# Kernel tuning notes

Measured on AMD Instinct MI355X. Metric: run time of the kernel, lower is better.

## Reference

```python
import jax, jax.numpy as jnp
import numpy as np

N_ATOMS = 32768
N_EDGES = 262144
ATOM_F = 256
EDGE_F = 128
OUT_F = 512
N_GAUSS = 50
SPIN_D = 3


def setup_inputs() -> dict:
    key = jax.random.key(0)
    k1, k2, k3, k4, k5 = jax.random.split(key, 5)
    h = jax.random.normal(k1, (N_ATOMS, ATOM_F), dtype=jnp.float32)
    m = jax.random.normal(k2, (N_EDGES, EDGE_F), dtype=jnp.float32)
    magft_cat = jax.random.normal(k3, (N_ATOMS, SPIN_D), dtype=jnp.float32)
    edge_index = jax.random.randint(k4, (2, N_EDGES), 0, N_ATOMS, dtype=jnp.int64)
    in_f = 2 * ATOM_F + EDGE_F + N_GAUSS  # 690
    W = jax.random.normal(k5, (OUT_F, in_f), dtype=jnp.float32) * 0.02
    return {"h": h, "m": m, "magft_cat": magft_cat, "edge_index": edge_index, "W": W}


def reference(h, m, magft_cat, edge_index, W):
    # GaussianSmearing(-1.5, 1.5, 50)
    offsets = jnp.linspace(-1.5, 1.5, N_GAUSS, dtype=jnp.float32)  # (G,)
    coeff = -0.5 / (offsets[1] - offsets[0]) ** 2

    src = edge_index[0]
    tgt = edge_index[1]
    h_s = h[src]                     # (E, A)
    h_t = h[tgt]                     # (E, A)
    # per-edge spin dot product, (E, 1)
    d = jnp.sum(magft_cat[src] * magft_cat[tgt], axis=1, keepdims=True)
    spin_edge = jnp.exp(coeff * (d - offsets) ** 2)  # (E, G)
    m_st = jnp.concatenate([h_s, h_t, m, spin_edge], axis=-1)  # (E, 690)
    # bias-free Dense with activation=None
    return m_st @ W.T  # (E, OUT_F)
```

## Files before the change

kernel.cpp:

```cpp
#include <hip/hip_runtime.h>
#include <hip/hip_bf16.h>

#define N_ATOMS 32768
#define N_EDGESC 262144
#define ATOM_F 256
#define EDGE_F 128
#define OUT_F 512
#define N_GAUSS 50
#define IN_F 690
#define NCHUNK 11

#define BM 128
#define BN 512
#define NTHREADS 512

using f32x4  = __attribute__((ext_vector_type(4))) float;
using short8 = __attribute__((ext_vector_type(8))) short;

__device__ __forceinline__ unsigned short f2bf(float f) {
  unsigned int u = __builtin_bit_cast(unsigned int, f);
  u += 0x7fffu + ((u >> 16) & 1u);
  return (unsigned short)(u >> 16);
}

__global__ void detect_idx_kernel(const unsigned int* __restrict__ ei, int* __restrict__ flag) {
  if (threadIdx.x == 0) {
    int ok = 1;
    for (int i = 0; i < 64; ++i) {
      unsigned int lo = ei[2 * i], hi = ei[2 * i + 1];
      if (hi != 0u || lo >= (unsigned)N_ATOMS) { ok = 0; break; }
    }
    *flag = ok;
  }
}

__global__ void prep_w_kernel(const float* __restrict__ W, unsigned short* __restrict__ Wp) {
  int g = blockIdx.x * blockDim.x + threadIdx.x;
  if (g >= NCHUNK * 2 * 32 * 64) return;
  int l  = g & 63;
  int nt = (g >> 6) & 31;
  int ks = (g >> 11) & 1;
  int kc = g >> 12;
  int n  = nt * 16 + (l & 15);
  int k0 = kc * 64 + ks * 32 + ((l >> 4) << 3);
  unsigned int u[4];
#pragma unroll
  for (int p = 0; p < 4; ++p) {
    int ka = k0 + 2 * p, kb = k0 + 2 * p + 1;
    float va = (ka < IN_F) ? W[n * IN_F + ka] : 0.0f;
    float vb = (kb < IN_F) ? W[n * IN_F + kb] : 0.0f;
    u[p] = (unsigned)f2bf(va) | ((unsigned)f2bf(vb) << 16);
  }
  *(uint4*)(Wp + (size_t)g * 8) = make_uint4(u[0], u[1], u[2], u[3]);
}

__global__ __launch_bounds__(NTHREADS, 2) void gemm_kernel(
    const float* __restrict__ h, const float* __restrict__ m,
    const float* __restrict__ magft, const void* __restrict__ ei,
    const int* __restrict__ flagp, const unsigned short* __restrict__ Wp,
    float* __restrict__ out)
{
  __shared__ __align__(16) unsigned short As[2][BM * 64];
  __shared__ int sIdx[BM], tIdx[BM];
  __shared__ float dLDS[BM];

  const int tid = threadIdx.x;
  const int eb  = blockIdx.x * BM;

  const int use64 = *flagp;
  if (tid < BM) {
    int e = eb + tid;
    int s, tg;
    if (use64) {
      const long long* p = (const long long*)ei;
      s  = (int)p[e];
      tg = (int)p[N_EDGESC + e];
    } else {
      const int* p = (const int*)ei;
      s  = p[e];
      tg = p[N_EDGESC + e];
    }
    sIdx[tid] = s;
    tIdx[tid] = tg;
    float ax = magft[3 * s],  ay = magft[3 * s + 1],  az = magft[3 * s + 2];
    float bx = magft[3 * tg], by = magft[3 * tg + 1], bz = magft[3 * tg + 2];
    dLDS[tid] = ax * bx + ay * by + az * bz;
  }
  __syncthreads();

  const int lane = tid & 63;
  const int wid  = tid >> 6;
  const int wr   = wid >> 2;
  const int wc   = wid & 3;

  const int ar = tid >> 2;
  const int aq = tid & 3;

  auto stageA = [&](int kchunk, int buf) {
    char* base = (char*)&As[buf][0] + ar * 128;
    const int sw = (ar & 7) << 4;
    if (kchunk < 10) {
      const float* p;
      if (kchunk < 8) {
        int atom = (kchunk < 4) ? sIdx[ar] : tIdx[ar];
        p = h + (size_t)atom * ATOM_F + (kchunk & 3) * 64 + aq * 16;
      } else {
        p = m + (size_t)(eb + ar) * EDGE_F + (kchunk & 1) * 64 + aq * 16;
      }
      float4 v[4];
#pragma unroll
      for (int j = 0; j < 4; ++j) v[j] = ((const float4*)p)[j];
      unsigned int u[8];
#pragma unroll
      for (int j = 0; j < 4; ++j) {
        u[2 * j]     = (unsigned)f2bf(v[j].x) | ((unsigned)f2bf(v[j].y) << 16);
        u[2 * j + 1] = (unsigned)f2bf(v[j].z) | ((unsigned)f2bf(v[j].w) << 16);
      }
      *(uint4*)(base + ((aq * 32)      ^ sw)) = make_uint4(u[0], u[1], u[2], u[3]);
      *(uint4*)(base + ((aq * 32 + 16) ^ sw)) = make_uint4(u[4], u[5], u[6], u[7]);
    } else {
      float d = dLDS[ar];
      const float step  = 3.0f / 49.0f;
      const float coeff = -0.5f / (step * step);
      unsigned int u[8];
#pragma unroll
      for (int p2 = 0; p2 < 8; ++p2) {
        int c0 = aq * 16 + 2 * p2, c1 = c0 + 1;
        float o0 = -1.5f + step * (float)c0;
        float o1 = -1.5f + step * (float)c1;
        float v0 = (c0 < N_GAUSS) ? __expf(coeff * (d - o0) * (d - o0)) : 0.0f;
        float v1 = (c1 < N_GAUSS) ? __expf(coeff * (d - o1) * (d - o1)) : 0.0f;
        u[p2] = (unsigned)f2bf(v0) | ((unsigned)f2bf(v1) << 16);
      }
      *(uint4*)(base + ((aq * 32)      ^ sw)) = make_uint4(u[0], u[1], u[2], u[3]);
      *(uint4*)(base + ((aq * 32 + 16) ^ sw)) = make_uint4(u[4], u[5], u[6], u[7]);
    }
  };

  f32x4 acc[4][8];
#pragma unroll
  for (int i = 0; i < 4; ++i)
#pragma unroll
    for (int j = 0; j < 8; ++j) acc[i][j] = (f32x4){0.f, 0.f, 0.f, 0.f};

  stageA(0, 0);
  __syncthreads();

  const short8* Wp8 = (const short8*)Wp;

  for (int kc = 0; kc < NCHUNK; ++kc) {
    const int cur = kc & 1;
    if (kc < NCHUNK - 1) stageA(kc + 1, cur ^ 1);

    const char* abase = (const char*)&As[cur][0];
#pragma unroll
    for (int ks = 0; ks < 2; ++ks) {
      short8 b[8];
#pragma unroll
      for (int ni = 0; ni < 8; ++ni)
        b[ni] = Wp8[(size_t)(((kc * 2 + ks) * 32 + wc * 8 + ni) << 6) + lane];
      short8 a[4];
#pragma unroll
      for (int mi = 0; mi < 4; ++mi) {
        int row = wr * 64 + mi * 16 + (lane & 15);
        int colb = (ks * 64 + ((lane >> 4) << 4)) ^ ((row & 7) << 4);
        a[mi] = *(const short8*)(abase + row * 128 + colb);
      }
#pragma unroll
      for (int mi = 0; mi < 4; ++mi)
#pragma unroll
        for (int ni = 0; ni < 8; ++ni)
          acc[mi][ni] = __builtin_amdgcn_mfma_f32_16x16x32_bf16(a[mi], b[ni], acc[mi][ni], 0, 0, 0);
    }
    if (kc < NCHUNK - 1) __syncthreads();
  }

#pragma unroll
  for (int mi = 0; mi < 4; ++mi) {
    int row0 = eb + wr * 64 + mi * 16 + ((lane >> 4) << 2);
#pragma unroll
    for (int ni = 0; ni < 8; ++ni) {
      int col = wc * 128 + ni * 16 + (lane & 15);
#pragma unroll
      for (int j = 0; j < 4; ++j) {
        out[(size_t)(row0 + j) * OUT_F + col] = acc[mi][ni][j];
      }
    }
  }
}

extern "C" void kernel_launch(void* const* d_in, const int* in_sizes, int n_in,
                              void* d_out, int out_size, void* d_ws, size_t ws_size,
                              hipStream_t stream) {
  const float* h     = (const float*)d_in[0];
  const float* m     = (const float*)d_in[1];
  const float* magft = (const float*)d_in[2];
  const void*  ei    = d_in[3];
  const float* W     = (const float*)d_in[4];
  float* out = (float*)d_out;

  char* ws = (char*)d_ws;
  int* flag = (int*)ws;
  unsigned short* Wp = (unsigned short*)(ws + 256);

  detect_idx_kernel<<<1, 64, 0, stream>>>((const unsigned int*)ei, flag);
  prep_w_kernel<<<(NCHUNK * 2 * 32 * 64 + 255) / 256, 256, 0, stream>>>(W, Wp);

  gemm_kernel<<<dim3(N_EDGESC / BM), NTHREADS, 0, stream>>>(h, m, magft, ei, flag, Wp, out);
}
```

Before: 311.7 us.

## Shrink GEMM tile to 64x256 with 2D grid and split A-stage load/write

The output tile shrinks from 128x512 to 64x256, the grid becomes two-dimensional over N and M, and there are 256 threads with a launch bound of 3 blocks per CU. The A staging is split into a global-load phase issued before the MFMA loop and an LDS-write phase after it, so gather latency overlaps compute. This is meant to cut accumulator registers and raise occupancy. In exchange, each edge row's gather, bf16 conversion and Gaussian expansion are now done twice, once per N-tile, which doubles A-side gather traffic.

```diff
diff --git a/kernel.cpp b/kernel.cpp
--- a/kernel.cpp
+++ b/kernel.cpp
@@ -10,9 +10,9 @@
 #define IN_F 690
 #define NCHUNK 11
 
-#define BM 128
-#define BN 512
-#define NTHREADS 512
+#define BM 64
+#define BN 256
+#define NTHREADS 256
 
 using f32x4  = __attribute__((ext_vector_type(4))) float;
 using short8 = __attribute__((ext_vector_type(8))) short;
@@ -54,7 +54,7 @@
   *(uint4*)(Wp + (size_t)g * 8) = make_uint4(u[0], u[1], u[2], u[3]);
 }
 
-__global__ __launch_bounds__(NTHREADS, 2) void gemm_kernel(
+__global__ __launch_bounds__(NTHREADS, 3) void gemm_kernel(
     const float* __restrict__ h, const float* __restrict__ m,
     const float* __restrict__ magft, const void* __restrict__ ei,
     const int* __restrict__ flagp, const unsigned short* __restrict__ Wp,
@@ -65,7 +65,8 @@
   __shared__ float dLDS[BM];
 
   const int tid = threadIdx.x;
-  const int eb  = blockIdx.x * BM;
+  const int eb  = blockIdx.y * BM;
+  const int ntb = blockIdx.x * 16;
 
   const int use64 = *flagp;
   if (tid < BM) {
@@ -89,16 +90,14 @@
   __syncthreads();
 
   const int lane = tid & 63;
-  const int wid  = tid >> 6;
-  const int wr   = wid >> 2;
-  const int wc   = wid & 3;
+  const int wc   = tid >> 6;
 
   const int ar = tid >> 2;
   const int aq = tid & 3;
 
-  auto stageA = [&](int kchunk, int buf) {
-    char* base = (char*)&As[buf][0] + ar * 128;
-    const int sw = (ar & 7) << 4;
+  float4 v[4];
+
+  auto stage_load = [&](int kchunk) {
     if (kchunk < 10) {
       const float* p;
       if (kchunk < 8) {
@@ -107,80 +106,86 @@
       } else {
         p = m + (size_t)(eb + ar) * EDGE_F + (kchunk & 1) * 64 + aq * 16;
       }
-      float4 v[4];
 #pragma unroll
       for (int j = 0; j < 4; ++j) v[j] = ((const float4*)p)[j];
-      unsigned int u[8];
-#pragma unroll
-      for (int j = 0; j < 4; ++j) {
-        u[2 * j]     = (unsigned)f2bf(v[j].x) | ((unsigned)f2bf(v[j].y) << 16);
-        u[2 * j + 1] = (unsigned)f2bf(v[j].z) | ((unsigned)f2bf(v[j].w) << 16);
-      }
-      *(uint4*)(base + ((aq * 32)      ^ sw)) = make_uint4(u[0], u[1], u[2], u[3]);
-      *(uint4*)(base + ((aq * 32 + 16) ^ sw)) = make_uint4(u[4], u[5], u[6], u[7]);
     } else {
       float d = dLDS[ar];
       const float step  = 3.0f / 49.0f;
       const float coeff = -0.5f / (step * step);
-      unsigned int u[8];
-#pragma unroll
-      for (int p2 = 0; p2 < 8; ++p2) {
-        int c0 = aq * 16 + 2 * p2, c1 = c0 + 1;
-        float o0 = -1.5f + step * (float)c0;
-        float o1 = -1.5f + step * (float)c1;
-        float v0 = (c0 < N_GAUSS) ? __expf(coeff * (d - o0) * (d - o0)) : 0.0f;
-        float v1 = (c1 < N_GAUSS) ? __expf(coeff * (d - o1) * (d - o1)) : 0.0f;
-        u[p2] = (unsigned)f2bf(v0) | ((unsigned)f2bf(v1) << 16);
-      }
-      *(uint4*)(base + ((aq * 32)      ^ sw)) = make_uint4(u[0], u[1], u[2], u[3]);
-      *(uint4*)(base + ((aq * 32 + 16) ^ sw)) = make_uint4(u[4], u[5], u[6], u[7]);
+#pragma unroll
+      for (int j = 0; j < 4; ++j) {
+#pragma unroll
+        for (int t = 0; t < 4; ++t) {
+          int c = aq * 16 + j * 4 + t;
+          float o = -1.5f + step * (float)c;
+          v[j][t] = (c < N_GAUSS) ? __expf(coeff * (d - o) * (d - o)) : 0.0f;
+        }
+      }
     }
   };
 
-  f32x4 acc[4][8];
+  auto stage_write = [&](int buf) {
+    unsigned int u[8];
+#pragma unroll
+    for (int j = 0; j < 4; ++j) {
+      u[2 * j]     = (unsigned)f2bf(v[j].x) | ((unsigned)f2bf(v[j].y) << 16);
+      u[2 * j + 1] = (unsigned)f2bf(v[j].z) | ((unsigned)f2bf(v[j].w) << 16);
+    }
+    char* base = (char*)&As[buf][0] + ar * 128;
+    const int sw = (ar & 7) << 4;
+    *(uint4*)(base + ((aq * 32)      ^ sw)) = make_uint4(u[0], u[1], u[2], u[3]);
+    *(uint4*)(base + ((aq * 32 + 16) ^ sw)) = make_uint4(u[4], u[5], u[6], u[7]);
+  };
+
+  f32x4 acc[4][4];
 #pragma unroll
   for (int i = 0; i < 4; ++i)
 #pragma unroll
-    for (int j = 0; j < 8; ++j) acc[i][j] = (f32x4){0.f, 0.f, 0.f, 0.f};
-
-  stageA(0, 0);
+    for (int j = 0; j < 4; ++j) acc[i][j] = (f32x4){0.f, 0.f, 0.f, 0.f};
+
+  stage_load(0);
+  stage_write(0);
   __syncthreads();
 
   const short8* Wp8 = (const short8*)Wp;
 
   for (int kc = 0; kc < NCHUNK; ++kc) {
     const int cur = kc & 1;
-    if (kc < NCHUNK - 1) stageA(kc + 1, cur ^ 1);
+    if (kc < NCHUNK - 1) stage_load(kc + 1);
 
     const char* abase = (const char*)&As[cur][0];
 #pragma unroll
     for (int ks = 0; ks < 2; ++ks) {
-      short8 b[8];
-#pragma unroll
-      for (int ni = 0; ni < 8; ++ni)
-        b[ni] = Wp8[(size_t)(((kc * 2 + ks) * 32 + wc * 8 + ni) << 6) + lane];
+      short8 b[4];
+#pragma unroll
+      for (int ni = 0; ni < 4; ++ni)
+        b[ni] = Wp8[(size_t)(((kc * 2 + ks) * 32 + ntb + wc * 4 + ni) << 6) + lane];
       short8 a[4];
 #pragma unroll
       for (int mi = 0; mi < 4; ++mi) {
-        int row = wr * 64 + mi * 16 + (lane & 15);
+        int row = mi * 16 + (lane & 15);
         int colb = (ks * 64 + ((lane >> 4) << 4)) ^ ((row & 7) << 4);
         a[mi] = *(const short8*)(abase + row * 128 + colb);
       }
 #pragma unroll
       for (int mi = 0; mi < 4; ++mi)
 #pragma unroll
-        for (int ni = 0; ni < 8; ++ni)
+        for (int ni = 0; ni < 4; ++ni)
           acc[mi][ni] = __builtin_amdgcn_mfma_f32_16x16x32_bf16(a[mi], b[ni], acc[mi][ni], 0, 0, 0);
     }
-    if (kc < NCHUNK - 1) __syncthreads();
+
+    if (kc < NCHUNK - 1) {
+      stage_write(cur ^ 1);
+      __syncthreads();
+    }
   }
 
 #pragma unroll
   for (int mi = 0; mi < 4; ++mi) {
-    int row0 = eb + wr * 64 + mi * 16 + ((lane >> 4) << 2);
-#pragma unroll
-    for (int ni = 0; ni < 8; ++ni) {
-      int col = wc * 128 + ni * 16 + (lane & 15);
+    int row0 = eb + mi * 16 + ((lane >> 4) << 2);
+#pragma unroll
+    for (int ni = 0; ni < 4; ++ni) {
+      int col = ntb * 16 + wc * 64 + ni * 16 + (lane & 15);
 #pragma unroll
       for (int j = 0; j < 4; ++j) {
         out[(size_t)(row0 + j) * OUT_F + col] = acc[mi][ni][j];
@@ -206,5 +211,5 @@
   detect_idx_kernel<<<1, 64, 0, stream>>>((const unsigned int*)ei, flag);
   prep_w_kernel<<<(NCHUNK * 2 * 32 * 64 + 255) / 256, 256, 0, stream>>>(W, Wp);
 
-  gemm_kernel<<<dim3(N_EDGESC / BM), NTHREADS, 0, stream>>>(h, m, magft, ei, flag, Wp, out);
-}
+  gemm_kernel<<<dim3(OUT_F / BN, N_EDGESC / BM), NTHREADS, 0, stream>>>(h, m, magft, ei, flag, Wp, out);
+}
```

Result: slower. 346.8 us (+11.3%).

## Pre-convert h to bf16, gather via global_load_lds, split N, triple-buffer

Applied to the files above, without the earlier changes.

A new kernel converts h to bf16 once. The GEMM then gathers the h rows straight into LDS with global_load_lds, so each gathered row no longer needs fp32 loads and per-element conversion in registers. The N dimension is split into two 256-wide halves, with block ids interleaved so both halves of the same edge tile run close together, and occupancy is raised to 4 blocks per CU. Staging moves to a 3-buffer pipeline, and s_setprio is raised around the MFMAs. In exchange there is an extra prep pass over h, the gather and m/spin staging work is duplicated across the two N halves, and the swizzle must stay consistent with the row-based LDS layout.

```diff
diff --git a/kernel.cpp b/kernel.cpp
--- a/kernel.cpp
+++ b/kernel.cpp
@@ -11,7 +11,7 @@
 #define NCHUNK 11
 
 #define BM 128
-#define BN 512
+#define BN 256
 #define NTHREADS 512
 
 using f32x4  = __attribute__((ext_vector_type(4))) float;
@@ -32,6 +32,19 @@
     }
     *flag = ok;
   }
+}
+
+__global__ void prep_h_kernel(const float* __restrict__ h, unsigned short* __restrict__ hb) {
+  size_t i = (size_t)(blockIdx.x * blockDim.x + threadIdx.x) * 8;
+  if (i >= (size_t)N_ATOMS * ATOM_F) return;
+  float4 a = *(const float4*)(h + i);
+  float4 b = *(const float4*)(h + i + 4);
+  uint4 o;
+  o.x = (unsigned)f2bf(a.x) | ((unsigned)f2bf(a.y) << 16);
+  o.y = (unsigned)f2bf(a.z) | ((unsigned)f2bf(a.w) << 16);
+  o.z = (unsigned)f2bf(b.x) | ((unsigned)f2bf(b.y) << 16);
+  o.w = (unsigned)f2bf(b.z) | ((unsigned)f2bf(b.w) << 16);
+  *(uint4*)(hb + i) = o;
 }
 
 __global__ void prep_w_kernel(const float* __restrict__ W, unsigned short* __restrict__ Wp) {
@@ -54,31 +67,34 @@
   *(uint4*)(Wp + (size_t)g * 8) = make_uint4(u[0], u[1], u[2], u[3]);
 }
 
-__global__ __launch_bounds__(NTHREADS, 2) void gemm_kernel(
-    const float* __restrict__ h, const float* __restrict__ m,
+__global__ __launch_bounds__(NTHREADS, 4) void gemm_kernel(
+    const unsigned short* __restrict__ hb, const float* __restrict__ m,
     const float* __restrict__ magft, const void* __restrict__ ei,
     const int* __restrict__ flagp, const unsigned short* __restrict__ Wp,
     float* __restrict__ out)
 {
-  __shared__ __align__(16) unsigned short As[2][BM * 64];
+  __shared__ __align__(16) unsigned short As[3][BM * 64];
   __shared__ int sIdx[BM], tIdx[BM];
   __shared__ float dLDS[BM];
 
   const int tid = threadIdx.x;
-  const int eb  = blockIdx.x * BM;
+  const int bid = blockIdx.x;
+  const int e  = (bid & 7) | ((bid >> 4) << 3);
+  const int nh = (bid >> 3) & 1;
+  const int eb = e * BM;
 
   const int use64 = *flagp;
   if (tid < BM) {
-    int e = eb + tid;
+    int ed = eb + tid;
     int s, tg;
     if (use64) {
       const long long* p = (const long long*)ei;
-      s  = (int)p[e];
-      tg = (int)p[N_EDGESC + e];
+      s  = (int)p[ed];
+      tg = (int)p[N_EDGESC + ed];
     } else {
       const int* p = (const int*)ei;
-      s  = p[e];
-      tg = p[N_EDGESC + e];
+      s  = p[ed];
+      tg = p[N_EDGESC + ed];
     }
     sIdx[tid] = s;
     tIdx[tid] = tg;
@@ -93,72 +109,80 @@
   const int wr   = wid >> 2;
   const int wc   = wid & 3;
 
+  const int r0 = wid * 16 + (lane >> 3);
+  const int hs0 = sIdx[r0], hs1 = sIdx[r0 + 8];
+  const int ht0 = tIdx[r0], ht1 = tIdx[r0 + 8];
+  const int srcsw = (((lane & 7) ^ (lane >> 3)) << 4);
+
   const int ar = tid >> 2;
   const int aq = tid & 3;
 
-  auto stageA = [&](int kchunk, int buf) {
-    char* base = (char*)&As[buf][0] + ar * 128;
-    const int sw = (ar & 7) << 4;
-    if (kchunk < 10) {
-      const float* p;
-      if (kchunk < 8) {
-        int atom = (kchunk < 4) ? sIdx[ar] : tIdx[ar];
-        p = h + (size_t)atom * ATOM_F + (kchunk & 3) * 64 + aq * 16;
+  auto stage = [&](int kchunk, int buf) {
+    if (kchunk < 8) {
+      int a0 = (kchunk < 4) ? hs0 : ht0;
+      int a1 = (kchunk < 4) ? hs1 : ht1;
+      const char* s0 = (const char*)hb + ((size_t)a0 * ATOM_F + (kchunk & 3) * 64) * 2 + srcsw;
+      const char* s1 = (const char*)hb + ((size_t)a1 * ATOM_F + (kchunk & 3) * 64) * 2 + srcsw;
+      char* d0 = (char*)&As[buf][0] + wid * 2048;
+      __builtin_amdgcn_global_load_lds(
+          (const __attribute__((address_space(1))) void*)s0,
+          (__attribute__((address_space(3))) void*)d0, 16, 0, 0);
+      __builtin_amdgcn_global_load_lds(
+          (const __attribute__((address_space(1))) void*)s1,
+          (__attribute__((address_space(3))) void*)(d0 + 1024), 16, 0, 0);
+    } else {
+      unsigned int u[8];
+      if (kchunk < 10) {
+        const float* p = m + (size_t)(eb + ar) * EDGE_F + (kchunk & 1) * 64 + aq * 16;
+        float4 v0 = ((const float4*)p)[0], v1 = ((const float4*)p)[1];
+        float4 v2 = ((const float4*)p)[2], v3 = ((const float4*)p)[3];
+        u[0] = (unsigned)f2bf(v0.x) | ((unsigned)f2bf(v0.y) << 16);
+        u[1] = (unsigned)f2bf(v0.z) | ((unsigned)f2bf(v0.w) << 16);
+        u[2] = (unsigned)f2bf(v1.x) | ((unsigned)f2bf(v1.y) << 16);
+        u[3] = (unsigned)f2bf(v1.z) | ((unsigned)f2bf(v1.w) << 16);
+        u[4] = (unsigned)f2bf(v2.x) | ((unsigned)f2bf(v2.y) << 16);
+        u[5] = (unsigned)f2bf(v2.z) | ((unsigned)f2bf(v2.w) << 16);
+        u[6] = (unsigned)f2bf(v3.x) | ((unsigned)f2bf(v3.y) << 16);
+        u[7] = (unsigned)f2bf(v3.z) | ((unsigned)f2bf(v3.w) << 16);
       } else {
-        p = m + (size_t)(eb + ar) * EDGE_F + (kchunk & 1) * 64 + aq * 16;
-      }
-      float4 v[4];
-#pragma unroll
-      for (int j = 0; j < 4; ++j) v[j] = ((const float4*)p)[j];
-      unsigned int u[8];
-#pragma unroll
-      for (int j = 0; j < 4; ++j) {
-        u[2 * j]     = (unsigned)f2bf(v[j].x) | ((unsigned)f2bf(v[j].y) << 16);
-        u[2 * j + 1] = (unsigned)f2bf(v[j].z) | ((unsigned)f2bf(v[j].w) << 16);
-      }
+        float d = dLDS[ar];
+        const float step  = 3.0f / 49.0f;
+        const float coeff = -0.5f / (step * step);
+#pragma unroll
+        for (int p2 = 0; p2 < 8; ++p2) {
+          int c0 = aq * 16 + 2 * p2, c1 = c0 + 1;
+          float o0 = -1.5f + step * (float)c0;
+          float o1 = -1.5f + step * (float)c1;
+          float w0 = (c0 < N_GAUSS) ? __expf(coeff * (d - o0) * (d - o0)) : 0.0f;
+          float w1 = (c1 < N_GAUSS) ? __expf(coeff * (d - o1) * (d - o1)) : 0.0f;
+          u[p2] = (unsigned)f2bf(w0) | ((unsigned)f2bf(w1) << 16);
+        }
+      }
+      char* base = (char*)&As[buf][0] + ar * 128;
+      const int sw = (ar & 7) << 4;
       *(uint4*)(base + ((aq * 32)      ^ sw)) = make_uint4(u[0], u[1], u[2], u[3]);
       *(uint4*)(base + ((aq * 32 + 16) ^ sw)) = make_uint4(u[4], u[5], u[6], u[7]);
-    } else {
-      float d = dLDS[ar];
-      const float step  = 3.0f / 49.0f;
-      const float coeff = -0.5f / (step * step);
-      unsigned int u[8];
-#pragma unroll
-      for (int p2 = 0; p2 < 8; ++p2) {
-        int c0 = aq * 16 + 2 * p2, c1 = c0 + 1;
-        float o0 = -1.5f + step * (float)c0;
-        float o1 = -1.5f + step * (float)c1;
-        float v0 = (c0 < N_GAUSS) ? __expf(coeff * (d - o0) * (d - o0)) : 0.0f;
-        float v1 = (c1 < N_GAUSS) ? __expf(coeff * (d - o1) * (d - o1)) : 0.0f;
-        u[p2] = (unsigned)f2bf(v0) | ((unsigned)f2bf(v1) << 16);
-      }
-      *(uint4*)(base + ((aq * 32)      ^ sw)) = make_uint4(u[0], u[1], u[2], u[3]);
-      *(uint4*)(base + ((aq * 32 + 16) ^ sw)) = make_uint4(u[4], u[5], u[6], u[7]);
     }
   };
 
-  f32x4 acc[4][8];
+  f32x4 acc[4][4];
 #pragma unroll
   for (int i = 0; i < 4; ++i)
 #pragma unroll
-    for (int j = 0; j < 8; ++j) acc[i][j] = (f32x4){0.f, 0.f, 0.f, 0.f};
-
-  stageA(0, 0);
-  __syncthreads();
+    for (int j = 0; j < 4; ++j) acc[i][j] = (f32x4){0.f, 0.f, 0.f, 0.f};
 
   const short8* Wp8 = (const short8*)Wp;
 
-  for (int kc = 0; kc < NCHUNK; ++kc) {
-    const int cur = kc & 1;
-    if (kc < NCHUNK - 1) stageA(kc + 1, cur ^ 1);
-
-    const char* abase = (const char*)&As[cur][0];
+  auto compute = [&](int kc, int buf) {
+    const char* abase = (const char*)&As[buf][0];
 #pragma unroll
     for (int ks = 0; ks < 2; ++ks) {
-      short8 b[8];
-#pragma unroll
-      for (int ni = 0; ni < 8; ++ni)
-        b[ni] = Wp8[(size_t)(((kc * 2 + ks) * 32 + wc * 8 + ni) << 6) + lane];
+      short8 b[4];
+#pragma unroll
+      for (int ni = 0; ni < 4; ++ni) {
+        int nt = nh * 16 + wc * 4 + ni;
+        b[ni] = Wp8[(size_t)(((kc * 2 + ks) * 32 + nt) << 6) + lane];
+      }
       short8 a[4];
 #pragma unroll
       for (int mi = 0; mi < 4; ++mi) {
@@ -166,21 +190,32 @@
         int colb = (ks * 64 + ((lane >> 4) << 4)) ^ ((row & 7) << 4);
         a[mi] = *(const short8*)(abase + row * 128 + colb);
       }
+      __builtin_amdgcn_s_setprio(1);
 #pragma unroll
       for (int mi = 0; mi < 4; ++mi)
 #pragma unroll
-        for (int ni = 0; ni < 8; ++ni)
+        for (int ni = 0; ni < 4; ++ni)
           acc[mi][ni] = __builtin_amdgcn_mfma_f32_16x16x32_bf16(a[mi], b[ni], acc[mi][ni], 0, 0, 0);
-    }
-    if (kc < NCHUNK - 1) __syncthreads();
+      __builtin_amdgcn_s_setprio(0);
+    }
+  };
+
+  stage(0, 0);
+  stage(1, 1);
+  __syncthreads();
+
+  for (int kc = 0; kc < NCHUNK; ++kc) {
+    if (kc + 2 < NCHUNK) stage(kc + 2, (kc + 2) % 3);
+    compute(kc, kc % 3);
+    if (kc + 1 < NCHUNK) __syncthreads();
   }
 
 #pragma unroll
   for (int mi = 0; mi < 4; ++mi) {
     int row0 = eb + wr * 64 + mi * 16 + ((lane >> 4) << 2);
 #pragma unroll
-    for (int ni = 0; ni < 8; ++ni) {
-      int col = wc * 128 + ni * 16 + (lane & 15);
+    for (int ni = 0; ni < 4; ++ni) {
+      int col = nh * 256 + wc * 64 + ni * 16 + (lane & 15);
 #pragma unroll
       for (int j = 0; j < 4; ++j) {
         out[(size_t)(row0 + j) * OUT_F + col] = acc[mi][ni][j];
@@ -202,9 +237,11 @@
   char* ws = (char*)d_ws;
   int* flag = (int*)ws;
   unsigned short* Wp = (unsigned short*)(ws + 256);
+  unsigned short* hb = (unsigned short*)(ws + 256 + 720896);
 
   detect_idx_kernel<<<1, 64, 0, stream>>>((const unsigned int*)ei, flag);
   prep_w_kernel<<<(NCHUNK * 2 * 32 * 64 + 255) / 256, 256, 0, stream>>>(W, Wp);
-
-  gemm_kernel<<<dim3(N_EDGESC / BM), NTHREADS, 0, stream>>>(h, m, magft, ei, flag, Wp, out);
-}
+  prep_h_kernel<<<(N_ATOMS * ATOM_F / 8 + 255) / 256, 256, 0, stream>>>(h, hb);
+
+  gemm_kernel<<<dim3(2 * N_EDGESC / BM), NTHREADS, 0, stream>>>(hb, m, magft, ei, flag, Wp, out);
+}
```

Result: slower. 328.3 us (+5.3%).
